# Performance work log

Hardware: AMD Instinct MI355X
Metric: run time of the kernel (lower is better)

The kernel has to match this reference:

```python
import jax, jax.numpy as jnp
import numpy as np

B, OBS, HID, LAT, OUT, E, NB, K = 4096, 1024, 1024, 512, 19, 8, 3, 2
EPS = float(np.finfo(float).eps)


def _resnet(x, W1, b1, W2, b2, Wf, bf):
    # W1:[NB,in,hid] b1:[NB,hid] W2:[NB,hid,in] b2:[NB,in] Wf:[in,out] bf:[out]
    def step(h, p):
        w1, bb1, w2, bb2 = p
        return h + jnp.maximum(h @ w1 + bb1, 0.0) @ w2 + bb2, None
    x, _ = jax.lax.scan(step, x, (W1, b1, W2, b2))
    return x @ Wf + bf


def setup_inputs() -> dict:
    key = jax.random.key(0)
    ks = jax.random.split(key, 16)
    s = 0.02
    def init(k, shape):
        return jax.random.normal(k, shape, jnp.float32) * s
    return {
        "obs": jax.random.normal(ks[0], (B, OBS), jnp.float32),
        # encoder ResNet: obs -> latent
        "enc_W1": init(ks[1], (NB, OBS, HID)), "enc_b1": jnp.zeros((NB, HID), jnp.float32),
        "enc_W2": init(ks[2], (NB, HID, OBS)), "enc_b2": jnp.zeros((NB, OBS), jnp.float32),
        "enc_Wf": init(ks[3], (OBS, LAT)), "enc_bf": jnp.zeros((LAT,), jnp.float32),
        # E stacked expert ResNets: latent -> out
        "exp_W1": init(ks[4], (E, NB, LAT, HID)), "exp_b1": jnp.zeros((E, NB, HID), jnp.float32),
        "exp_W2": init(ks[5], (E, NB, HID, LAT)), "exp_b2": jnp.zeros((E, NB, LAT), jnp.float32),
        "exp_Wf": init(ks[6], (E, LAT, OUT)), "exp_bf": jnp.zeros((E, OUT), jnp.float32),
        # value ResNet: obs -> 1
        "val_W1": init(ks[7], (NB, OBS, HID)), "val_b1": jnp.zeros((NB, HID), jnp.float32),
        "val_W2": init(ks[8], (NB, HID, OBS)), "val_b2": jnp.zeros((NB, OBS), jnp.float32),
        "val_Wf": init(ks[9], (OBS, 1)), "val_bf": jnp.zeros((1,), jnp.float32),
        # gate (torch init is zeros; use random for a non-degenerate test)
        "w_gate": init(ks[10], (LAT, E)),
    }


def reference(obs, enc_W1, enc_b1, enc_W2, enc_b2, enc_Wf, enc_bf,
              exp_W1, exp_b1, exp_W2, exp_b2, exp_Wf, exp_bf,
              val_W1, val_b1, val_W2, val_b2, val_Wf, val_bf, w_gate):
    latent = _resnet(obs, enc_W1, enc_b1, enc_W2, enc_b2, enc_Wf, enc_bf)  # [B,LAT]
    # top-k gating (noisy_gating=False): softmax over the k selected logits
    logits = latent @ w_gate                                   # [B,E]
    top_vals, top_idx = jax.lax.top_k(logits, K)               # [B,K]
    top_g = jax.nn.softmax(top_vals, axis=-1)
    gates = jnp.zeros_like(logits).at[jnp.arange(logits.shape[0])[:, None], top_idx].set(top_g)
    # per-expert ResNet on all tokens; zero gates null out non-dispatched tokens
    expert_out = jax.vmap(lambda w1, b1, w2, b2, wf, bf:
                          _resnet(latent, w1, b1, w2, b2, wf, bf))(
        exp_W1, exp_b1, exp_W2, exp_b2, exp_Wf, exp_bf)        # [E,B,OUT]
    y = jnp.einsum('ebo,be->bo', expert_out, gates)            # weighted combine
    y = jnp.where(y == 0.0, EPS, y)                            # SparseDispatcher.combine quirk
    v = _resnet(obs, val_W1, val_b1, val_W2, val_b2, val_Wf, val_bf)  # [B,1]
    return jnp.concatenate([y, v], axis=-1)                    # [B,OUT+1]
```

## Files before the change

kernel.cpp:

```cpp
#include <hip/hip_runtime.h>
#include <hip/hip_bf16.h>
#include <stdint.h>
#include <stddef.h>

typedef __hip_bfloat16 bf16;
typedef __attribute__((ext_vector_type(8))) short short8;
typedef __attribute__((ext_vector_type(4))) float f32x4;

#define GLDS16(g, l) __builtin_amdgcn_global_load_lds( \
    (const __attribute__((address_space(1))) void*)(g), \
    (__attribute__((address_space(3))) void*)(l), 16, 0, 0)

__device__ __forceinline__ float bf2f(bf16 x) { return __bfloat162float(x); }
__device__ __forceinline__ bf16  f2bf(float x) { return __float2bfloat16(x); }

constexpr int CAP = 4096;

template<bool SPLIT>
__global__ void wconv(const float* __restrict__ src, bf16* __restrict__ dhi,
                      bf16* __restrict__ dlo, int K, int N) {
  __shared__ float tile[32][33];
  const size_t zoff = (size_t)blockIdx.z * K * N;
  const float* s = src + zoff;
  const int n0 = blockIdx.x * 32, k0 = blockIdx.y * 32;
  const int tx = threadIdx.x & 31, ty = threadIdx.x >> 5;
#pragma unroll
  for (int i = 0; i < 32; i += 8)
    tile[ty + i][tx] = s[(size_t)(k0 + ty + i) * N + (n0 + tx)];
  __syncthreads();
#pragma unroll
  for (int i = 0; i < 32; i += 8) {
    const float v = tile[tx][ty + i];
    const size_t o = zoff + (size_t)(n0 + ty + i) * K + (k0 + tx);
    const bf16 h = f2bf(v);
    dhi[o] = h;
    if (SPLIT) dlo[o] = f2bf(v - bf2f(h));
  }
}

__global__ void splitv(const float* __restrict__ x, bf16* __restrict__ hi,
                       bf16* __restrict__ lo, int n4) {
  const int i = blockIdx.x * 256 + threadIdx.x;
  if (i >= n4) return;
  const float4 v = ((const float4*)x)[i];
  const float f[4] = {v.x, v.y, v.z, v.w};
#pragma unroll
  for (int j = 0; j < 4; ++j) {
    const bf16 h = f2bf(f[j]);
    hi[i * 4 + j] = h;
    lo[i * 4 + j] = f2bf(f[j] - bf2f(h));
  }
}

template<int EPI, bool SPLIT, bool GATHER>
__device__ __forceinline__ void gemm_tile(
    const bf16* __restrict__ Ah, const bf16* __restrict__ Al,
    const bf16* __restrict__ Bh, const bf16* __restrict__ Bl,
    const float* __restrict__ bias,
    const bf16* __restrict__ Rb, const bf16* __restrict__ Rl2,
    float* __restrict__ Cf, bf16* __restrict__ Ch, bf16* __restrict__ Cl,
    const int* __restrict__ permz, int cE,
    int bx, int by, int N, int K, int lda, int kbase,
    bf16* As, bf16* Bs) {
  const int tid = threadIdx.x, lane = tid & 63, wave = tid >> 6;
  const int wr = wave >> 1, wc = wave & 1;
  const int fr = lane & 15, q = lane >> 4, fq = q << 2;

  int arow[4], brow[4];
#pragma unroll
  for (int i = 0; i < 4; ++i) {
    const int r = (i * 256 + tid) >> 3;
    const int slot = bx * 128 + r;
    arow[i] = GATHER ? ((slot < cE) ? permz[slot] : 0) : slot;
    brow[i] = by * 128 + r;
  }

  f32x4 acc[4][4];
#pragma unroll
  for (int m = 0; m < 4; ++m)
#pragma unroll
    for (int n = 0; n < 4; ++n) {
      acc[m][n][0] = 0.f; acc[m][n][1] = 0.f; acc[m][n][2] = 0.f; acc[m][n][3] = 0.f;
    }

  const int nk = K >> 6;
  for (int kt = 0; kt < nk; ++kt) {
    const int k0 = kbase + (kt << 6);
#pragma unroll
    for (int i = 0; i < 4; ++i) {
      const int ci = i * 256 + tid;
      const int r = ci >> 3, pch = ci & 7;
      const int c = pch ^ (r & 7);
      const size_t ga = (size_t)arow[i] * lda + k0 + c * 8;
      const size_t gb = (size_t)brow[i] * lda + k0 + c * 8;
      GLDS16(Ah + ga, As + ci * 8);
      GLDS16(Bh + gb, Bs + ci * 8);
      if (SPLIT) {
        GLDS16(Al + ga, As + 8192 + ci * 8);
        GLDS16(Bl + gb, Bs + 8192 + ci * 8);
      }
    }
    __syncthreads();

#pragma unroll
    for (int kk = 0; kk < 2; ++kk) {
      auto LD = [&](const bf16* base, int r) -> short8 {
        const int c = ((kk << 2) + q) ^ (r & 7);
        return *(const short8*)(base + r * 64 + c * 8);
      };
      short8 a0[4], b0[4];
#pragma unroll
      for (int m = 0; m < 4; ++m) a0[m] = LD(As, wr * 64 + m * 16 + fr);
#pragma unroll
      for (int n = 0; n < 4; ++n) b0[n] = LD(Bs, wc * 64 + n * 16 + fr);
      if (SPLIT) {
        short8 a1[4], b1[4];
#pragma unroll
        for (int m = 0; m < 4; ++m) a1[m] = LD(As + 8192, wr * 64 + m * 16 + fr);
#pragma unroll
        for (int n = 0; n < 4; ++n) b1[n] = LD(Bs + 8192, wc * 64 + n * 16 + fr);
#pragma unroll
        for (int m = 0; m < 4; ++m)
#pragma unroll
          for (int n = 0; n < 4; ++n) {
            acc[m][n] = __builtin_amdgcn_mfma_f32_16x16x32_bf16(a1[m], b0[n], acc[m][n], 0, 0, 0);
            acc[m][n] = __builtin_amdgcn_mfma_f32_16x16x32_bf16(a0[m], b1[n], acc[m][n], 0, 0, 0);
          }
      }
#pragma unroll
      for (int m = 0; m < 4; ++m)
#pragma unroll
        for (int n = 0; n < 4; ++n)
          acc[m][n] = __builtin_amdgcn_mfma_f32_16x16x32_bf16(a0[m], b0[n], acc[m][n], 0, 0, 0);
    }
    __syncthreads();
  }

#pragma unroll
  for (int n = 0; n < 4; ++n) {
    const int col = by * 128 + wc * 64 + n * 16 + fr;
    const float bv = (EPI == 6) ? 0.f : bias[col];
#pragma unroll
    for (int m = 0; m < 4; ++m) {
      const int row0 = bx * 128 + wr * 64 + m * 16 + fq;
#pragma unroll
      for (int r = 0; r < 4; ++r) {
        const int rowi = row0 + r;
        const size_t o = (size_t)rowi * N + col;
        float v = acc[m][n][r] + bv;
        if (EPI == 0 || EPI == 3) v = fmaxf(v, 0.f);
        if (EPI == 1) v += bf2f(Rb[o]) + bf2f(Rl2[o]);
        if (EPI == 4) v += bf2f(Rb[o]);
        if (EPI == 5) {
          const int rr = (rowi < cE) ? permz[rowi] : 0;
          v += bf2f(Rb[(size_t)rr * N + col]);
        }
        if (EPI == 6) {
          Cf[o] = v;
        } else {
          const bf16 h = f2bf(v);
          Ch[o] = h;
          if (EPI == 0 || EPI == 1) Cl[o] = f2bf(v - bf2f(h));
        }
      }
    }
  }
}

template<int EPI, bool SPLIT, bool GATHER, bool SPLITK>
__global__ __launch_bounds__(256, 2)
void gemm_bt(const bf16* __restrict__ Ah, const bf16* __restrict__ Al, size_t aSz,
             const bf16* __restrict__ Bh, const bf16* __restrict__ Bl, size_t bSz,
             const float* __restrict__ bias, size_t biasSz,
             const void* __restrict__ R, size_t rSz,
             float* __restrict__ Cf, bf16* __restrict__ Ch, bf16* __restrict__ Cl, size_t cSz,
             const int* __restrict__ perm, const int* __restrict__ cnt,
             int M, int N, int K, int lda) {
  __shared__ __align__(16) bf16 As[(SPLIT ? 2 : 1) * 8192];
  __shared__ __align__(16) bf16 Bs[(SPLIT ? 2 : 1) * 8192];
  const int gx = M >> 7, gy = N >> 7, nwg = gridDim.x, lid = blockIdx.x;
  const int wid = (lid & 7) * (nwg >> 3) + (lid >> 3);
  const int by = wid % gy, bx = (wid / gy) % gx, bz = wid / (gy * gx);

  int cE = 0x7fffffff;
  if (cnt) { cE = cnt[bz]; if (bx * 128 >= cE) return; }

  Ah += (size_t)bz * aSz;
  Bh += (size_t)bz * bSz;
  if (SPLIT) { Al += (size_t)bz * aSz; Bl += (size_t)bz * bSz; }
  if (bias) bias += (size_t)bz * biasSz;
  const bf16* Rb = (const bf16*)R;
  if (EPI == 4) Rb += (size_t)bz * rSz;
  if (EPI == 6) Cf += (size_t)bz * cSz; else Ch += (size_t)bz * cSz;
  const int* permz = perm ? (perm + (size_t)bz * CAP) : nullptr;
  const int kbase = SPLITK ? bz * K : 0;

  gemm_tile<EPI, SPLIT, GATHER>(Ah, Al, Bh, Bl, bias, Rb, nullptr, Cf, Ch, Cl,
                                permz, cE, bx, by, N, K, lda, kbase, As, Bs);
}

template<int EPI0, int EPI1>
__global__ __launch_bounds__(256, 2)
void gemm_dual(const bf16* __restrict__ Ah, const bf16* __restrict__ Al,
               const bf16* __restrict__ B0h, const bf16* __restrict__ B0l,
               const float* __restrict__ bias0,
               const bf16* __restrict__ R0h, const bf16* __restrict__ R0l,
               bf16* __restrict__ C0h, bf16* __restrict__ C0l,
               const bf16* __restrict__ A1, const bf16* __restrict__ B1,
               const float* __restrict__ bias1, const bf16* __restrict__ R1,
               bf16* __restrict__ C1,
               int M, int N, int K) {
  __shared__ __align__(16) bf16 As[2 * 8192];
  __shared__ __align__(16) bf16 Bs[2 * 8192];
  const int gy = N >> 7, nwg = gridDim.x, lid = blockIdx.x;
  const int wid = (lid & 7) * (nwg >> 3) + (lid >> 3);
  const int z = wid & 1, w2 = wid >> 1;
  const int by = w2 % gy, bx = w2 / gy;
  if (z == 0)
    gemm_tile<EPI0, true, false>(Ah, Al, B0h, B0l, bias0, R0h, R0l, nullptr, C0h, C0l,
                                 nullptr, 0x7fffffff, bx, by, N, K, K, 0, As, Bs);
  else
    gemm_tile<EPI1, false, false>(A1, nullptr, B1, nullptr, bias1, R1, nullptr, nullptr, C1, nullptr,
                                  nullptr, 0x7fffffff, bx, by, N, K, K, 0, As, Bs);
}

__global__ void gate_logits(const float* __restrict__ P0, const float* __restrict__ P1,
                            const float* __restrict__ bfv, const float* __restrict__ wg,
                            bf16* __restrict__ latB, int* __restrict__ tokE,
                            float2* __restrict__ tokG) {
  __shared__ float wgs[8 * 512];
  __shared__ float bfs[512];
  const int tid = threadIdx.x;
  for (int i = tid; i < 4096; i += 256) wgs[(i & 7) * 512 + (i >> 3)] = wg[i];
  for (int i = tid; i < 512; i += 256) bfs[i] = bfv[i];
  __syncthreads();
  const int lane = tid & 63, wv = tid >> 6;
#pragma unroll 1
  for (int tt = 0; tt < 4; ++tt) {
    const int t = blockIdx.x * 16 + wv * 4 + tt;
    float lv[8];
    float le[8] = {0.f, 0.f, 0.f, 0.f, 0.f, 0.f, 0.f, 0.f};
#pragma unroll
    for (int j = 0; j < 8; ++j) {
      const int k = lane + 64 * j;
      lv[j] = P0[(size_t)t * 512 + k] + P1[(size_t)t * 512 + k] + bfs[k];
      latB[(size_t)t * 512 + k] = f2bf(lv[j]);
#pragma unroll
      for (int e = 0; e < 8; ++e) le[e] = fmaf(lv[j], wgs[e * 512 + k], le[e]);
    }
#pragma unroll
    for (int e = 0; e < 8; ++e) {
#pragma unroll
      for (int d = 32; d > 0; d >>= 1) le[e] += __shfl_down(le[e], d);
    }
    if (lane == 0) {
      int i1 = 0; float v1 = le[0];
#pragma unroll
      for (int e = 1; e < 8; ++e) if (le[e] > v1) { v1 = le[e]; i1 = e; }
      int i2 = -1; float v2 = -3.4e38f;
#pragma unroll
      for (int e = 0; e < 8; ++e) if (e != i1 && le[e] > v2) { v2 = le[e]; i2 = e; }
      const float e2 = expf(v2 - v1);
      const float inv = 1.f / (1.f + e2);
      tokE[t] = i1 | (i2 << 8);
      tokG[t] = make_float2(inv, e2 * inv);
    }
  }
}

__global__ void gate_compact(const int* __restrict__ tokE, int* __restrict__ perm,
                             int* __restrict__ cnt, int* __restrict__ slot1,
                             int* __restrict__ slot2) {
  const int e = blockIdx.x;
  __shared__ int wsum[4];
  __shared__ int sbase;
  if (threadIdx.x == 0) sbase = 0;
  __syncthreads();
  const int lane = threadIdx.x & 63, wv = threadIdx.x >> 6;
  for (int c0 = 0; c0 < 4096; c0 += 256) {
    const int t = c0 + threadIdx.x;
    const int te = tokE[t];
    const int which = ((te & 255) == e) ? 0 : ((((te >> 8) & 255) == e) ? 1 : -1);
    const unsigned long long m = __ballot(which >= 0);
    if (lane == 0) wsum[wv] = __popcll(m);
    __syncthreads();
    int off = sbase;
    for (int w = 0; w < wv; ++w) off += wsum[w];
    if (which >= 0) {
      const int slot = off + __popcll(m & ((1ull << lane) - 1ull));
      perm[e * CAP + slot] = t;
      if (which == 0) slot1[t] = slot; else slot2[t] = slot;
    }
    __syncthreads();
    if (threadIdx.x == 0) sbase += wsum[0] + wsum[1] + wsum[2] + wsum[3];
    __syncthreads();
  }
  if (threadIdx.x == 0) cnt[e] = sbase;
}

__global__ void combine_out(const bf16* __restrict__ He, const float* __restrict__ Wf,
                            const float* __restrict__ Bf, const int* __restrict__ tokE,
                            const float2* __restrict__ tokG, const int* __restrict__ slot1,
                            const int* __restrict__ slot2, float* __restrict__ out) {
  const int b = blockIdx.x * 4 + (threadIdx.x >> 6);
  const int lane = threadIdx.x & 63;
  const int te = tokE[b];
  const float2 gg = tokG[b];
  const int ee[2] = {te & 255, (te >> 8) & 255};
  const int sl[2] = {slot1[b], slot2[b]};
  const float gv[2] = {gg.x, gg.y};
  float y[19];
#pragma unroll
  for (int o = 0; o < 19; ++o) y[o] = 0.f;
#pragma unroll
  for (int t = 0; t < 2; ++t) {
    const bf16* h = He + ((size_t)ee[t] * CAP + sl[t]) * 512;
    float part[19];
#pragma unroll
    for (int o = 0; o < 19; ++o) part[o] = 0.f;
    for (int k = lane; k < 512; k += 64) {
      const float hv = bf2f(h[k]);
      const float* w = Wf + ((size_t)ee[t] * 512 + k) * 19;
#pragma unroll
      for (int o = 0; o < 19; ++o) part[o] = fmaf(hv, w[o], part[o]);
    }
#pragma unroll
    for (int o = 0; o < 19; ++o) y[o] = fmaf(gv[t], part[o], y[o]);
  }
#pragma unroll
  for (int o = 0; o < 19; ++o) {
#pragma unroll
    for (int d = 32; d > 0; d >>= 1) y[o] += __shfl_down(y[o], d);
  }
  if (lane == 0) {
#pragma unroll
    for (int o = 0; o < 19; ++o) {
      float v = y[o] + gg.x * Bf[ee[0] * 19 + o] + gg.y * Bf[ee[1] * 19 + o];
      if (v == 0.f) v = 2.2204460492503131e-16f;
      out[(size_t)b * 20 + o] = v;
    }
  }
}

__global__ void value_out(const bf16* __restrict__ Hv, const float* __restrict__ Wf,
                          const float* __restrict__ Bf, float* __restrict__ out) {
  const int b = blockIdx.x * 4 + (threadIdx.x >> 6);
  const int lane = threadIdx.x & 63;
  const bf16* h = Hv + (size_t)b * 1024;
  float s = 0.f;
  for (int k = lane; k < 1024; k += 64) s = fmaf(bf2f(h[k]), Wf[k], s);
#pragma unroll
  for (int d = 32; d > 0; d >>= 1) s += __shfl_down(s, d);
  if (lane == 0) out[(size_t)b * 20 + 19] = s + Bf[0];
}

extern "C" void kernel_launch(void* const* d_in, const int* in_sizes, int n_in,
                              void* d_out, int out_size, void* d_ws, size_t ws_size,
                              hipStream_t stream) {
  (void)in_sizes; (void)n_in; (void)out_size; (void)ws_size;
  const int Btok = 4096;

  const float* obs   = (const float*)d_in[0];
  const float* encW1 = (const float*)d_in[1];
  const float* encB1 = (const float*)d_in[2];
  const float* encW2 = (const float*)d_in[3];
  const float* encB2 = (const float*)d_in[4];
  const float* encWf = (const float*)d_in[5];
  const float* encBf = (const float*)d_in[6];
  const float* expW1 = (const float*)d_in[7];
  const float* expB1 = (const float*)d_in[8];
  const float* expW2 = (const float*)d_in[9];
  const float* expB2 = (const float*)d_in[10];
  const float* expWf = (const float*)d_in[11];
  const float* expBf = (const float*)d_in[12];
  const float* valW1 = (const float*)d_in[13];
  const float* valB1 = (const float*)d_in[14];
  const float* valW2 = (const float*)d_in[15];
  const float* valB2 = (const float*)d_in[16];
  const float* valWf = (const float*)d_in[17];
  const float* valBf = (const float*)d_in[18];
  const float* wgate = (const float*)d_in[19];

  char* p = (char*)d_ws;
  auto alloc = [&](size_t bytes) -> char* {
    char* r = p; p += (bytes + 255) & ~(size_t)255; return r;
  };
  bf16* encW1tH = (bf16*)alloc((size_t)3 * 1024 * 1024 * 2);
  bf16* encW1tL = (bf16*)alloc((size_t)3 * 1024 * 1024 * 2);
  bf16* encW2tH = (bf16*)alloc((size_t)3 * 1024 * 1024 * 2);
  bf16* encW2tL = (bf16*)alloc((size_t)3 * 1024 * 1024 * 2);
  bf16* encWftH = (bf16*)alloc((size_t)512 * 1024 * 2);
  bf16* encWftL = (bf16*)alloc((size_t)512 * 1024 * 2);
  bf16* valW1t  = (bf16*)alloc((size_t)3 * 1024 * 1024 * 2);
  bf16* valW2t  = (bf16*)alloc((size_t)3 * 1024 * 1024 * 2);
  bf16* expW1t  = (bf16*)alloc((size_t)24 * 512 * 1024 * 2);
  bf16* expW2t  = (bf16*)alloc((size_t)24 * 512 * 1024 * 2);
  bf16*  obsH  = (bf16*)alloc((size_t)Btok * 1024 * 2);
  bf16*  tH    = (bf16*)alloc((size_t)Btok * 1024 * 2);
  bf16*  hH    = (bf16*)alloc((size_t)Btok * 1024 * 2);
  bf16*  vT    = (bf16*)alloc((size_t)Btok * 1024 * 2);
  bf16*  vH    = (bf16*)alloc((size_t)Btok * 1024 * 2);
  bf16*  latB  = (bf16*)alloc((size_t)Btok * 512 * 2);
  int*   perm  = (int*)alloc((size_t)8 * CAP * 4);
  int*   cnt   = (int*)alloc(8 * 4);
  int*   tokE  = (int*)alloc((size_t)Btok * 4);
  float2* tokG = (float2*)alloc((size_t)Btok * 8);
  int*   slot1 = (int*)alloc((size_t)Btok * 4);
  int*   slot2 = (int*)alloc((size_t)Btok * 4);
  char* heR = alloc((size_t)8 * CAP * 512 * 2);
  bf16* He   = (bf16*)heR;
  bf16* tL   = (bf16*)heR;
  bf16* hL   = (bf16*)(heR + (size_t)Btok * 1024 * 2);
  bf16* obsL = (bf16*)(heR + (size_t)2 * Btok * 1024 * 2);
  char* teR = alloc((size_t)8 * CAP * 1024 * 2);
  bf16*  Te = (bf16*)teR;
  float* P0 = (float*)teR;
  float* P1 = P0 + (size_t)Btok * 512;

  const dim3 blk(256);

  splitv<<<dim3((Btok * 1024 / 4 + 255) / 256), blk, 0, stream>>>(obs, obsH, obsL, Btok * 1024 / 4);
  wconv<true ><<<dim3(32, 32, 3),  blk, 0, stream>>>(encW1, encW1tH, encW1tL, 1024, 1024);
  wconv<true ><<<dim3(32, 32, 3),  blk, 0, stream>>>(encW2, encW2tH, encW2tL, 1024, 1024);
  wconv<true ><<<dim3(16, 32, 1),  blk, 0, stream>>>(encWf, encWftH, encWftL, 1024, 512);
  wconv<false><<<dim3(32, 32, 3),  blk, 0, stream>>>(valW1, valW1t, nullptr, 1024, 1024);
  wconv<false><<<dim3(32, 32, 3),  blk, 0, stream>>>(valW2, valW2t, nullptr, 1024, 1024);
  wconv<false><<<dim3(32, 16, 24), blk, 0, stream>>>(expW1, expW1t, nullptr, 512, 1024);
  wconv<false><<<dim3(16, 32, 24), blk, 0, stream>>>(expW2, expW2t, nullptr, 1024, 512);

  {
    const bf16 *aH = obsH, *aL = obsL, *rH = obsH, *rL = obsL;
    const bf16 *av = obsH, *rv = obsH;
    for (int bi = 0; bi < 3; ++bi) {
      gemm_dual<0, 3><<<dim3(512), blk, 0, stream>>>(
          aH, aL, encW1tH + (size_t)bi * 1024 * 1024, encW1tL + (size_t)bi * 1024 * 1024,
          encB1 + bi * 1024, nullptr, nullptr, tH, tL,
          av, valW1t + (size_t)bi * 1024 * 1024, valB1 + bi * 1024, nullptr, vT,
          Btok, 1024, 1024);
      gemm_dual<1, 4><<<dim3(512), blk, 0, stream>>>(
          tH, tL, encW2tH + (size_t)bi * 1024 * 1024, encW2tL + (size_t)bi * 1024 * 1024,
          encB2 + bi * 1024, rH, rL, hH, hL,
          vT, valW2t + (size_t)bi * 1024 * 1024, valB2 + bi * 1024, rv, vH,
          Btok, 1024, 1024);
      aH = hH; aL = hL; rH = hH; rL = hL;
      av = vH; rv = vH;
    }
  }

  gemm_bt<6, true, false, true><<<dim3(256), blk, 0, stream>>>(
      hH, hL, 0, encWftH, encWftL, 0, nullptr, 0, nullptr, 0,
      P0, nullptr, nullptr, (size_t)Btok * 512, nullptr, nullptr,
      Btok, 512, 512, 1024);

  gate_logits<<<dim3(256), blk, 0, stream>>>(P0, P1, encBf, wgate, latB, tokE, tokG);
  gate_compact<<<dim3(8), blk, 0, stream>>>(tokE, perm, cnt, slot1, slot2);

  {
    const size_t sW1 = (size_t)512 * 1024, sW2 = (size_t)1024 * 512;
    const size_t sTe = (size_t)CAP * 1024, sHe = (size_t)CAP * 512;
    for (int bi = 0; bi < 3; ++bi) {
      if (bi == 0) {
        gemm_bt<3, false, true, false><<<dim3(2048), blk, 0, stream>>>(
            latB, nullptr, 0, expW1t + bi * sW1, nullptr, 3 * sW1,
            expB1 + bi * 1024, 3 * 1024, nullptr, 0, nullptr, Te, nullptr, sTe,
            perm, cnt, CAP, 1024, 512, 512);
        gemm_bt<5, false, false, false><<<dim3(1024), blk, 0, stream>>>(
            Te, nullptr, sTe, expW2t + bi * sW2, nullptr, 3 * sW2,
            expB2 + bi * 512, 3 * 512, latB, 0, nullptr, He, nullptr, sHe,
            perm, cnt, CAP, 512, 1024, 1024);
      } else {
        gemm_bt<3, false, false, false><<<dim3(2048), blk, 0, stream>>>(
            He, nullptr, sHe, expW1t + bi * sW1, nullptr, 3 * sW1,
            expB1 + bi * 1024, 3 * 1024, nullptr, 0, nullptr, Te, nullptr, sTe,
            perm, cnt, CAP, 1024, 512, 512);
        gemm_bt<4, false, false, false><<<dim3(1024), blk, 0, stream>>>(
            Te, nullptr, sTe, expW2t + bi * sW2, nullptr, 3 * sW2,
            expB2 + bi * 512, 3 * 512, He, sHe, nullptr, He, nullptr, sHe,
            perm, cnt, CAP, 512, 1024, 1024);
      }
    }
  }
  combine_out<<<dim3(1024), blk, 0, stream>>>(He, expWf, expBf, tokE, tokG, slot1, slot2,
                                              (float*)d_out);
  value_out<<<dim3(1024), blk, 0, stream>>>(vH, valWf, valBf, (float*)d_out);
}
```

Before: 760.7 us.

## Halve GEMM K-tile to raise occupancy, batch weight conversions, widen split-K and compaction

```diff
diff --git a/kernel.cpp b/kernel.cpp
--- a/kernel.cpp
+++ b/kernel.cpp
@@ -16,25 +16,36 @@
 
 constexpr int CAP = 4096;
 
-template<bool SPLIT>
-__global__ void wconv(const float* __restrict__ src, bf16* __restrict__ dhi,
-                      bf16* __restrict__ dlo, int K, int N) {
+struct WJob { const float* src; bf16* dhi; bf16* dlo; int K, N, start; };
+struct WJobs { WJob j[7]; };
+
+__global__ void wconv_all(WJobs jobs) {
   __shared__ float tile[32][33];
-  const size_t zoff = (size_t)blockIdx.z * K * N;
-  const float* s = src + zoff;
-  const int n0 = blockIdx.x * 32, k0 = blockIdx.y * 32;
+  const int bid = blockIdx.x;
+  int ji = 0;
+#pragma unroll
+  for (int t = 1; t < 7; ++t) if (bid >= jobs.j[t].start) ji = t;
+  const WJob J = jobs.j[ji];
+  const int K = J.K, N = J.N;
+  const int nx = N >> 5, tps = nx * (K >> 5);
+  const int local = bid - J.start;
+  const int z = local / tps, rem = local % tps;
+  const int n0 = (rem % nx) * 32, k0 = (rem / nx) * 32;
+  const size_t zoff = (size_t)z * K * N;
+  const float* s = J.src + zoff;
   const int tx = threadIdx.x & 31, ty = threadIdx.x >> 5;
 #pragma unroll
   for (int i = 0; i < 32; i += 8)
     tile[ty + i][tx] = s[(size_t)(k0 + ty + i) * N + (n0 + tx)];
   __syncthreads();
+  const bool split = (J.dlo != nullptr);
 #pragma unroll
   for (int i = 0; i < 32; i += 8) {
     const float v = tile[tx][ty + i];
     const size_t o = zoff + (size_t)(n0 + ty + i) * K + (k0 + tx);
     const bf16 h = f2bf(v);
-    dhi[o] = h;
-    if (SPLIT) dlo[o] = f2bf(v - bf2f(h));
+    J.dhi[o] = h;
+    if (split) J.dlo[o] = f2bf(v - bf2f(h));
   }
 }
 
@@ -66,10 +77,10 @@
   const int wr = wave >> 1, wc = wave & 1;
   const int fr = lane & 15, q = lane >> 4, fq = q << 2;
 
-  int arow[4], brow[4];
-#pragma unroll
-  for (int i = 0; i < 4; ++i) {
-    const int r = (i * 256 + tid) >> 3;
+  int arow[2], brow[2];
+#pragma unroll
+  for (int i = 0; i < 2; ++i) {
+    const int r = (i * 256 + tid) >> 2;
     const int slot = bx * 128 + r;
     arow[i] = GATHER ? ((slot < cE) ? permz[slot] : 0) : slot;
     brow[i] = by * 128 + r;
@@ -83,56 +94,53 @@
       acc[m][n][0] = 0.f; acc[m][n][1] = 0.f; acc[m][n][2] = 0.f; acc[m][n][3] = 0.f;
     }
 
-  const int nk = K >> 6;
+  const int nk = K >> 5;
   for (int kt = 0; kt < nk; ++kt) {
-    const int k0 = kbase + (kt << 6);
-#pragma unroll
-    for (int i = 0; i < 4; ++i) {
+    const int k0 = kbase + (kt << 5);
+#pragma unroll
+    for (int i = 0; i < 2; ++i) {
       const int ci = i * 256 + tid;
-      const int r = ci >> 3, pch = ci & 7;
-      const int c = pch ^ (r & 7);
+      const int r = ci >> 2, pch = ci & 3;
+      const int c = pch ^ ((r >> 1) & 3);
       const size_t ga = (size_t)arow[i] * lda + k0 + c * 8;
       const size_t gb = (size_t)brow[i] * lda + k0 + c * 8;
       GLDS16(Ah + ga, As + ci * 8);
       GLDS16(Bh + gb, Bs + ci * 8);
       if (SPLIT) {
-        GLDS16(Al + ga, As + 8192 + ci * 8);
-        GLDS16(Bl + gb, Bs + 8192 + ci * 8);
+        GLDS16(Al + ga, As + 4096 + ci * 8);
+        GLDS16(Bl + gb, Bs + 4096 + ci * 8);
       }
     }
     __syncthreads();
 
-#pragma unroll
-    for (int kk = 0; kk < 2; ++kk) {
-      auto LD = [&](const bf16* base, int r) -> short8 {
-        const int c = ((kk << 2) + q) ^ (r & 7);
-        return *(const short8*)(base + r * 64 + c * 8);
-      };
-      short8 a0[4], b0[4];
-#pragma unroll
-      for (int m = 0; m < 4; ++m) a0[m] = LD(As, wr * 64 + m * 16 + fr);
-#pragma unroll
-      for (int n = 0; n < 4; ++n) b0[n] = LD(Bs, wc * 64 + n * 16 + fr);
-      if (SPLIT) {
-        short8 a1[4], b1[4];
-#pragma unroll
-        for (int m = 0; m < 4; ++m) a1[m] = LD(As + 8192, wr * 64 + m * 16 + fr);
-#pragma unroll
-        for (int n = 0; n < 4; ++n) b1[n] = LD(Bs + 8192, wc * 64 + n * 16 + fr);
-#pragma unroll
-        for (int m = 0; m < 4; ++m)
-#pragma unroll
-          for (int n = 0; n < 4; ++n) {
-            acc[m][n] = __builtin_amdgcn_mfma_f32_16x16x32_bf16(a1[m], b0[n], acc[m][n], 0, 0, 0);
-            acc[m][n] = __builtin_amdgcn_mfma_f32_16x16x32_bf16(a0[m], b1[n], acc[m][n], 0, 0, 0);
-          }
-      }
+    auto LD = [&](const bf16* base, int r) -> short8 {
+      const int c = q ^ ((r >> 1) & 3);
+      return *(const short8*)(base + r * 32 + c * 8);
+    };
+    short8 a0[4], b0[4];
+#pragma unroll
+    for (int m = 0; m < 4; ++m) a0[m] = LD(As, wr * 64 + m * 16 + fr);
+#pragma unroll
+    for (int n = 0; n < 4; ++n) b0[n] = LD(Bs, wc * 64 + n * 16 + fr);
+    if (SPLIT) {
+      short8 a1[4], b1[4];
+#pragma unroll
+      for (int m = 0; m < 4; ++m) a1[m] = LD(As + 4096, wr * 64 + m * 16 + fr);
+#pragma unroll
+      for (int n = 0; n < 4; ++n) b1[n] = LD(Bs + 4096, wc * 64 + n * 16 + fr);
 #pragma unroll
       for (int m = 0; m < 4; ++m)
 #pragma unroll
-        for (int n = 0; n < 4; ++n)
-          acc[m][n] = __builtin_amdgcn_mfma_f32_16x16x32_bf16(a0[m], b0[n], acc[m][n], 0, 0, 0);
-    }
+        for (int n = 0; n < 4; ++n) {
+          acc[m][n] = __builtin_amdgcn_mfma_f32_16x16x32_bf16(a1[m], b0[n], acc[m][n], 0, 0, 0);
+          acc[m][n] = __builtin_amdgcn_mfma_f32_16x16x32_bf16(a0[m], b1[n], acc[m][n], 0, 0, 0);
+        }
+    }
+#pragma unroll
+    for (int m = 0; m < 4; ++m)
+#pragma unroll
+      for (int n = 0; n < 4; ++n)
+        acc[m][n] = __builtin_amdgcn_mfma_f32_16x16x32_bf16(a0[m], b0[n], acc[m][n], 0, 0, 0);
     __syncthreads();
   }
 
@@ -168,7 +176,7 @@
 }
 
 template<int EPI, bool SPLIT, bool GATHER, bool SPLITK>
-__global__ __launch_bounds__(256, 2)
+__global__ __launch_bounds__(256, 3)
 void gemm_bt(const bf16* __restrict__ Ah, const bf16* __restrict__ Al, size_t aSz,
              const bf16* __restrict__ Bh, const bf16* __restrict__ Bl, size_t bSz,
              const float* __restrict__ bias, size_t biasSz,
@@ -176,8 +184,8 @@
              float* __restrict__ Cf, bf16* __restrict__ Ch, bf16* __restrict__ Cl, size_t cSz,
              const int* __restrict__ perm, const int* __restrict__ cnt,
              int M, int N, int K, int lda) {
-  __shared__ __align__(16) bf16 As[(SPLIT ? 2 : 1) * 8192];
-  __shared__ __align__(16) bf16 Bs[(SPLIT ? 2 : 1) * 8192];
+  __shared__ __align__(16) bf16 As[(SPLIT ? 2 : 1) * 4096];
+  __shared__ __align__(16) bf16 Bs[(SPLIT ? 2 : 1) * 4096];
   const int gx = M >> 7, gy = N >> 7, nwg = gridDim.x, lid = blockIdx.x;
   const int wid = (lid & 7) * (nwg >> 3) + (lid >> 3);
   const int by = wid % gy, bx = (wid / gy) % gx, bz = wid / (gy * gx);
@@ -200,7 +208,7 @@
 }
 
 template<int EPI0, int EPI1>
-__global__ __launch_bounds__(256, 2)
+__global__ __launch_bounds__(256, 3)
 void gemm_dual(const bf16* __restrict__ Ah, const bf16* __restrict__ Al,
                const bf16* __restrict__ B0h, const bf16* __restrict__ B0l,
                const float* __restrict__ bias0,
@@ -210,8 +218,8 @@
                const float* __restrict__ bias1, const bf16* __restrict__ R1,
                bf16* __restrict__ C1,
                int M, int N, int K) {
-  __shared__ __align__(16) bf16 As[2 * 8192];
-  __shared__ __align__(16) bf16 Bs[2 * 8192];
+  __shared__ __align__(16) bf16 As[2 * 4096];
+  __shared__ __align__(16) bf16 Bs[2 * 4096];
   const int gy = N >> 7, nwg = gridDim.x, lid = blockIdx.x;
   const int wid = (lid & 7) * (nwg >> 3) + (lid >> 3);
   const int z = wid & 1, w2 = wid >> 1;
@@ -224,7 +232,7 @@
                                   nullptr, 0x7fffffff, bx, by, N, K, K, 0, As, Bs);
 }
 
-__global__ void gate_logits(const float* __restrict__ P0, const float* __restrict__ P1,
+__global__ void gate_logits(const float* __restrict__ P, size_t pstr,
                             const float* __restrict__ bfv, const float* __restrict__ wg,
                             bf16* __restrict__ latB, int* __restrict__ tokE,
                             float2* __restrict__ tokG) {
@@ -238,15 +246,15 @@
 #pragma unroll 1
   for (int tt = 0; tt < 4; ++tt) {
     const int t = blockIdx.x * 16 + wv * 4 + tt;
-    float lv[8];
     float le[8] = {0.f, 0.f, 0.f, 0.f, 0.f, 0.f, 0.f, 0.f};
 #pragma unroll
     for (int j = 0; j < 8; ++j) {
       const int k = lane + 64 * j;
-      lv[j] = P0[(size_t)t * 512 + k] + P1[(size_t)t * 512 + k] + bfs[k];
-      latB[(size_t)t * 512 + k] = f2bf(lv[j]);
-#pragma unroll
-      for (int e = 0; e < 8; ++e) le[e] = fmaf(lv[j], wgs[e * 512 + k], le[e]);
+      const size_t idx = (size_t)t * 512 + k;
+      const float lv = P[idx] + P[pstr + idx] + P[2 * pstr + idx] + P[3 * pstr + idx] + bfs[k];
+      latB[idx] = f2bf(lv);
+#pragma unroll
+      for (int e = 0; e < 8; ++e) le[e] = fmaf(lv, wgs[e * 512 + k], le[e]);
     }
 #pragma unroll
     for (int e = 0; e < 8; ++e) {
@@ -272,12 +280,12 @@
                              int* __restrict__ cnt, int* __restrict__ slot1,
                              int* __restrict__ slot2) {
   const int e = blockIdx.x;
-  __shared__ int wsum[4];
+  __shared__ int wsum[16];
   __shared__ int sbase;
   if (threadIdx.x == 0) sbase = 0;
   __syncthreads();
   const int lane = threadIdx.x & 63, wv = threadIdx.x >> 6;
-  for (int c0 = 0; c0 < 4096; c0 += 256) {
+  for (int c0 = 0; c0 < 4096; c0 += 1024) {
     const int t = c0 + threadIdx.x;
     const int te = tokE[t];
     const int which = ((te & 255) == e) ? 0 : ((((te >> 8) & 255) == e) ? 1 : -1);
@@ -292,7 +300,12 @@
       if (which == 0) slot1[t] = slot; else slot2[t] = slot;
     }
     __syncthreads();
-    if (threadIdx.x == 0) sbase += wsum[0] + wsum[1] + wsum[2] + wsum[3];
+    if (threadIdx.x == 0) {
+      int s = 0;
+#pragma unroll
+      for (int w = 0; w < 16; ++w) s += wsum[w];
+      sbase += s;
+    }
     __syncthreads();
   }
   if (threadIdx.x == 0) cnt[e] = sbase;
@@ -414,19 +427,26 @@
   bf16* obsL = (bf16*)(heR + (size_t)2 * Btok * 1024 * 2);
   char* teR = alloc((size_t)8 * CAP * 1024 * 2);
   bf16*  Te = (bf16*)teR;
-  float* P0 = (float*)teR;
-  float* P1 = P0 + (size_t)Btok * 512;
+  float* P  = (float*)teR;
+  const size_t pstr = (size_t)Btok * 512;
 
   const dim3 blk(256);
 
-  splitv<<<dim3((Btok * 1024 / 4 + 255) / 256), blk, 0, stream>>>(obs, obsH, obsL, Btok * 1024 / 4);
-  wconv<true ><<<dim3(32, 32, 3),  blk, 0, stream>>>(encW1, encW1tH, encW1tL, 1024, 1024);
-  wconv<true ><<<dim3(32, 32, 3),  blk, 0, stream>>>(encW2, encW2tH, encW2tL, 1024, 1024);
-  wconv<true ><<<dim3(16, 32, 1),  blk, 0, stream>>>(encWf, encWftH, encWftL, 1024, 512);
-  wconv<false><<<dim3(32, 32, 3),  blk, 0, stream>>>(valW1, valW1t, nullptr, 1024, 1024);
-  wconv<false><<<dim3(32, 32, 3),  blk, 0, stream>>>(valW2, valW2t, nullptr, 1024, 1024);
-  wconv<false><<<dim3(32, 16, 24), blk, 0, stream>>>(expW1, expW1t, nullptr, 512, 1024);
-  wconv<false><<<dim3(16, 32, 24), blk, 0, stream>>>(expW2, expW2t, nullptr, 1024, 512);
+  splitv<<<dim3(Btok * 1024 / 4 / 256), blk, 0, stream>>>(obs, obsH, obsL, Btok * 1024 / 4);
+  {
+    WJobs jb;
+    auto set = [&](int i, const float* s, bf16* dh, bf16* dl, int K, int N, int st) {
+      jb.j[i] = WJob{s, dh, dl, K, N, st};
+    };
+    set(0, encW1, encW1tH, encW1tL, 1024, 1024, 0);
+    set(1, encW2, encW2tH, encW2tL, 1024, 1024, 3072);
+    set(2, encWf, encWftH, encWftL, 1024, 512, 6144);
+    set(3, valW1, valW1t, nullptr, 1024, 1024, 6656);
+    set(4, valW2, valW2t, nullptr, 1024, 1024, 9728);
+    set(5, expW1, expW1t, nullptr, 512, 1024, 12800);
+    set(6, expW2, expW2t, nullptr, 1024, 512, 25088);
+    wconv_all<<<dim3(37376), blk, 0, stream>>>(jb);
+  }
 
   {
     const bf16 *aH = obsH, *aL = obsL, *rH = obsH, *rL = obsL;
@@ -447,13 +467,13 @@
     }
   }
 
-  gemm_bt<6, true, false, true><<<dim3(256), blk, 0, stream>>>(
+  gemm_bt<6, true, false, true><<<dim3(512), blk, 0, stream>>>(
       hH, hL, 0, encWftH, encWftL, 0, nullptr, 0, nullptr, 0,
-      P0, nullptr, nullptr, (size_t)Btok * 512, nullptr, nullptr,
-      Btok, 512, 512, 1024);
-
-  gate_logits<<<dim3(256), blk, 0, stream>>>(P0, P1, encBf, wgate, latB, tokE, tokG);
-  gate_compact<<<dim3(8), blk, 0, stream>>>(tokE, perm, cnt, slot1, slot2);
+      P, nullptr, nullptr, pstr, nullptr, nullptr,
+      Btok, 512, 256, 1024);
+
+  gate_logits<<<dim3(256), blk, 0, stream>>>(P, pstr, encBf, wgate, latB, tokE, tokG);
+  gate_compact<<<dim3(8), dim3(1024), 0, stream>>>(tokE, perm, cnt, slot1, slot2);
 
   {
     const size_t sW1 = (size_t)512 * 1024, sW2 = (size_t)1024 * 512;
```

Measured after the change: 827.3 us. +8.8%, slower.
